# Kernel optimization log

Hardware: AMD Instinct MI355X
Metric: run time of the kernel (lower is better)

The kernel has to match this reference:

```python
import jax, jax.numpy as jnp
import numpy as np

SIGMA_D = 1.0  # init kwarg sigma_d
# d_model = 2 -> div_term = exp(arange(0,2,2) * (-ln(10000)/2)) = [1.0]


def setup_inputs() -> dict:
    key = jax.random.key(0)
    k0, k1 = jax.random.split(key)
    B, N, M = 4, 3000, 3000
    points0 = jax.random.normal(k0, (B, N, 2), dtype=jnp.float32)
    points1 = jax.random.normal(k1, (B, M, 2), dtype=jnp.float32)
    return {"points0": points0, "points1": points1}


def reference(points0, points1):
    # pairwise distance with points_normlize=True: sq_dist = clamp(2 - 2*<p0,p1>, 0)
    xy = jnp.einsum('bnc,bmc->bnm', points0, points1)  # (B,N,M)
    sq_dist = jnp.clip(2.0 - 2.0 * xy, 0.0)
    d_indices = jnp.sqrt(sq_dist) / SIGMA_D  # (B,N,M)
    # sinusoidal embedding with d_model=2, div_term=[1.0] -> [sin(d), cos(d)]
    d_embeddings = jnp.stack([jnp.sin(d_indices), jnp.cos(d_indices)], axis=-1)  # (B,N,M,2)
    d_embeddings = jax.lax.stop_gradient(d_embeddings)  # torch detaches + no_grad
    # einsum 'bnc,bnmc->bnc': multiply by sum over m
    points0_emb = points0 * d_embeddings.sum(axis=2)  # (B,N,2)
    # einsum 'bmc,bmnc->bmc' with permuted emb: sum over n
    points1_emb = points1 * d_embeddings.sum(axis=1)  # (B,M,2)
    return (points0_emb, points1_emb)
```

## Files before the change

### kernel.cpp

```cpp
#include <hip/hip_runtime.h>
#include <math.h>


#define GB 4
#define GN 3000
#define RB 32
#define BLKS 94
#define HALF 1500
#define K2 0.025330295910584444f
#define C2 0.050660591821168888f

#define COLPART_F2 (GB*BLKS*GN)

__device__ __forceinline__ float sreg(float x) {
    return __int_as_float(__builtin_amdgcn_readfirstlane(__float_as_int(x)));
}

__global__ __launch_bounds__(256, 4) void geo_pair_kernel(
    const float* __restrict__ p0,
    const float* __restrict__ p1,
    float2* __restrict__ ws)
{
    __shared__ float2 cp[4][768];

    const int lane = threadIdx.x & 63;
    const int wv   = threadIdx.x >> 6;
    const int h    = blockIdx.x & 1;
    const int t    = blockIdx.x >> 1;
    const int b    = t / BLKS;
    const int blk  = t - b * BLKS;
    const int row0 = blk * RB + wv * 8;
    const bool active = (row0 < GN);

    float s[8], c[8], ax[8], ay[8];
    float2 pr[8];
    #pragma unroll
    for (int r = 0; r < 8; ++r) {
        s[r] = 0.f; c[r] = 0.f; ax[r] = 0.f; ay[r] = 0.f;
        pr[r] = make_float2(0.f, 0.f);
    }
    const float2* __restrict__ qp = (const float2*)p1;
    float2 qA = make_float2(0.f, 0.f), qB = qA;
    const float c2v = C2;

    if (active) {
        const float2* ownp = (const float2*)p0 + b * GN + row0;
        const float mm = -2.0f * K2;
        #pragma unroll
        for (int r = 0; r < 8; ++r) {
            pr[r] = ownp[r];
            ax[r] = sreg(mm * pr[r].x);
            ay[r] = sreg(mm * pr[r].y);
        }
        qp = (const float2*)p1 + b * GN + h * HALF + lane;
        qA = qp[0];
        qB = qp[64];
    } else {
        for (int i = lane; i < 768; i += 64)
            cp[wv][i] = make_float2(0.f, 0.f);
    }

    float2* cw = &cp[wv][lane];

#define STEP(q) do {                                                         \
    float sn[8], cs[8];                                                      \
    _Pragma("unroll")                                                        \
    for (int r = 0; r < 8; ++r) {                                            \
        float tt = fmaf(ax[r], (q).x, fmaf(ay[r], (q).y, c2v));              \
        tt = fmaxf(tt, 0.f);                                                 \
        float rr = __builtin_amdgcn_sqrtf(tt);                               \
        sn[r] = __builtin_amdgcn_sinf(rr);                                   \
        cs[r] = __builtin_amdgcn_cosf(rr);                                   \
        s[r] += sn[r]; c[r] += cs[r];                                        \
    }                                                                        \
    float ssum = ((sn[0]+sn[1]) + (sn[2]+sn[3]))                             \
               + ((sn[4]+sn[5]) + (sn[6]+sn[7]));                            \
    float csum = ((cs[0]+cs[1]) + (cs[2]+cs[3]))                             \
               + ((cs[4]+cs[5]) + (cs[6]+cs[7]));                            \
    cw[0] = make_float2(ssum, csum);                                         \
    cw += 64;                                                                \
} while (0)

    if (active) {
        #pragma unroll 1
        for (int js = 0; js < 10; ++js) {
            float2 qC = qp[128];
            qp += 64;
            STEP(qA);
            qA = qB; qB = qC;
        }
        STEP(qA);
        STEP(qB);
        qA = qp[128];
        qB = qp[192];
        qp += 128;
    }
    __syncthreads();
    float2* __restrict__ dst = ws + (b * BLKS + blk) * GN + h * HALF;
    for (int i = threadIdx.x; i < 768; i += 256) {
        float2 a0 = cp[0][i], a1 = cp[1][i], a2 = cp[2][i], a3 = cp[3][i];
        dst[i] = make_float2((a0.x + a1.x) + (a2.x + a3.x),
                             (a0.y + a1.y) + (a2.y + a3.y));
    }
    __syncthreads();

    cw = &cp[wv][lane];
    if (active) {
        #pragma unroll 1
        for (int js = 0; js < 9; ++js) {
            float2 qC = qp[128];
            qp += 64;
            STEP(qA);
            qA = qB; qB = qC;
        }
        STEP(qA);
        STEP(qB);
        if (lane < 28) {
            float2 qT = qp[128];
            STEP(qT);
        }
    }
    __syncthreads();
    for (int i = threadIdx.x; i < 732; i += 256) {
        float2 a0 = cp[0][i], a1 = cp[1][i], a2 = cp[2][i], a3 = cp[3][i];
        dst[768 + i] = make_float2((a0.x + a1.x) + (a2.x + a3.x),
                                   (a0.y + a1.y) + (a2.y + a3.y));
    }
#undef STEP

    if (active) {
        #pragma unroll
        for (int off = 32; off >= 1; off >>= 1) {
            #pragma unroll
            for (int r = 0; r < 8; ++r) {
                s[r] += __shfl_down(s[r], off, 64);
                c[r] += __shfl_down(c[r], off, 64);
            }
        }
        if (lane == 0) {
            float2* rp = ws + COLPART_F2 + ((b * GN + row0) << 1) + h;
            #pragma unroll
            for (int r = 0; r < 8; ++r)
                rp[r * 2] = make_float2(s[r], c[r]);
        }
    }
}

__global__ __launch_bounds__(256, 4) void geo_reduce_kernel(
    const float* __restrict__ p0,
    const float* __restrict__ p1,
    const float2* __restrict__ ws,
    float2* __restrict__ out)
{
    __shared__ float2 acc[8][32];
    const int blk = blockIdx.x;
    if (blk < 375) {
        const int cc = threadIdx.x & 31;
        const int kc = threadIdx.x >> 5;
        const int g  = blk * 32 + cc;
        const int b  = g / GN;
        const int m  = g - b * GN;
        const float2* __restrict__ base = ws + b * (BLKS * GN) + m;
        const int k0 = kc * 12;
        float sv = 0.f, cv = 0.f;
        #pragma unroll
        for (int j = 0; j < 12; ++j) {
            const int k = k0 + j;
            if (k < BLKS) {
                float2 v = base[k * GN];
                sv += v.x; cv += v.y;
            }
        }
        acc[kc][cc] = make_float2(sv, cv);
        __syncthreads();
        if (kc == 0) {
            float2 r = acc[0][cc];
            #pragma unroll
            for (int j = 1; j < 8; ++j) { r.x += acc[j][cc].x; r.y += acc[j][cc].y; }
            const float2 p = ((const float2*)p1)[g];
            out[GB * GN + g] = make_float2(p.x * r.x, p.y * r.y);
        }
    } else {
        const int r = (blk - 375) * 256 + threadIdx.x;
        if (r < GB * GN) {
            const float2* rp = ws + COLPART_F2 + (r << 1);
            const float2 a = rp[0], d = rp[1];
            const float2 p = ((const float2*)p0)[r];
            out[r] = make_float2(p.x * (a.x + d.x), p.y * (a.y + d.y));
        }
    }
}

extern "C" void kernel_launch(void* const* d_in, const int* in_sizes, int n_in,
                              void* d_out, int out_size, void* d_ws, size_t ws_size,
                              hipStream_t stream) {
    const float* points0 = (const float*)d_in[0];
    const float* points1 = (const float*)d_in[1];

    geo_pair_kernel<<<dim3(GB * BLKS * 2), dim3(256), 0, stream>>>(
        points0, points1, (float2*)d_ws);
    geo_reduce_kernel<<<dim3(375 + 47), dim3(256), 0, stream>>>(
        points0, points1, (const float2*)d_ws, (float2*)d_out);
}
```

Baseline: 80.51 us.

## Write per-wave column partials directly to global, dropping LDS block reduction

Each wave now stores its per-column sin/cos partial sums straight to the workspace instead of combining the four waves of a block through shared memory with barriers. Inactive waves exit early. The reduce kernel now sums 375 row-group partials per column instead of 94. This removes the LDS traffic and syncthreads from the pair kernel, at the cost of about four times more workspace writes and reads in the reduction pass.

```diff
diff --git a/kernel.cpp b/kernel.cpp
--- a/kernel.cpp
+++ b/kernel.cpp
@@ -4,13 +4,13 @@
 
 #define GB 4
 #define GN 3000
-#define RB 32
+#define HALF 1500
+#define RGPB 375
 #define BLKS 94
-#define HALF 1500
 #define K2 0.025330295910584444f
 #define C2 0.050660591821168888f
 
-#define COLPART_F2 (GB*BLKS*GN)
+#define COLPART_F2 (GB*RGPB*GN)
 
 __device__ __forceinline__ float sreg(float x) {
     return __int_as_float(__builtin_amdgcn_readfirstlane(__float_as_int(x)));
@@ -21,48 +21,36 @@
     const float* __restrict__ p1,
     float2* __restrict__ ws)
 {
-    __shared__ float2 cp[4][768];
-
     const int lane = threadIdx.x & 63;
     const int wv   = threadIdx.x >> 6;
     const int h    = blockIdx.x & 1;
     const int t    = blockIdx.x >> 1;
     const int b    = t / BLKS;
     const int blk  = t - b * BLKS;
-    const int row0 = blk * RB + wv * 8;
-    const bool active = (row0 < GN);
+    const int rg   = blk * 4 + wv;
+    if (rg >= RGPB) return;
+    const int row0 = rg * 8;
 
     float s[8], c[8], ax[8], ay[8];
-    float2 pr[8];
-    #pragma unroll
-    for (int r = 0; r < 8; ++r) {
-        s[r] = 0.f; c[r] = 0.f; ax[r] = 0.f; ay[r] = 0.f;
-        pr[r] = make_float2(0.f, 0.f);
-    }
-    const float2* __restrict__ qp = (const float2*)p1;
-    float2 qA = make_float2(0.f, 0.f), qB = qA;
-    const float c2v = C2;
-
-    if (active) {
+    {
         const float2* ownp = (const float2*)p0 + b * GN + row0;
         const float mm = -2.0f * K2;
         #pragma unroll
         for (int r = 0; r < 8; ++r) {
-            pr[r] = ownp[r];
-            ax[r] = sreg(mm * pr[r].x);
-            ay[r] = sreg(mm * pr[r].y);
+            float2 pr = ownp[r];
+            ax[r] = sreg(mm * pr.x);
+            ay[r] = sreg(mm * pr.y);
+            s[r] = 0.f; c[r] = 0.f;
         }
-        qp = (const float2*)p1 + b * GN + h * HALF + lane;
-        qA = qp[0];
-        qB = qp[64];
-    } else {
-        for (int i = lane; i < 768; i += 64)
-            cp[wv][i] = make_float2(0.f, 0.f);
     }
+    const float c2v = C2;
 
-    float2* cw = &cp[wv][lane];
+    const float2* __restrict__ qp = (const float2*)p1 + b * GN + h * HALF + lane;
+    float2* __restrict__ sp = ws + (b * RGPB + rg) * GN + h * HALF + lane;
+    float2 qA = qp[0];
+    float2 qB = qp[64];
 
-#define STEP(q) do {                                                         \
+#define STEP(q, stoff) do {                                                  \
     float sn[8], cs[8];                                                      \
     _Pragma("unroll")                                                        \
     for (int r = 0; r < 8; ++r) {                                            \
@@ -77,72 +65,38 @@
                + ((sn[4]+sn[5]) + (sn[6]+sn[7]));                            \
     float csum = ((cs[0]+cs[1]) + (cs[2]+cs[3]))                             \
                + ((cs[4]+cs[5]) + (cs[6]+cs[7]));                            \
-    cw[0] = make_float2(ssum, csum);                                         \
-    cw += 64;                                                                \
+    sp[stoff] = make_float2(ssum, csum);                                     \
 } while (0)
 
-    if (active) {
-        #pragma unroll 1
-        for (int js = 0; js < 10; ++js) {
-            float2 qC = qp[128];
-            qp += 64;
-            STEP(qA);
-            qA = qB; qB = qC;
-        }
-        STEP(qA);
-        STEP(qB);
-        qA = qp[128];
-        qB = qp[192];
-        qp += 128;
+    #pragma unroll 1
+    for (int j = 0; j < 21; ++j) {
+        float2 qC = qp[128];
+        qp += 64;
+        STEP(qA, 0);
+        sp += 64;
+        qA = qB; qB = qC;
     }
-    __syncthreads();
-    float2* __restrict__ dst = ws + (b * BLKS + blk) * GN + h * HALF;
-    for (int i = threadIdx.x; i < 768; i += 256) {
-        float2 a0 = cp[0][i], a1 = cp[1][i], a2 = cp[2][i], a3 = cp[3][i];
-        dst[i] = make_float2((a0.x + a1.x) + (a2.x + a3.x),
-                             (a0.y + a1.y) + (a2.y + a3.y));
-    }
-    __syncthreads();
-
-    cw = &cp[wv][lane];
-    if (active) {
-        #pragma unroll 1
-        for (int js = 0; js < 9; ++js) {
-            float2 qC = qp[128];
-            qp += 64;
-            STEP(qA);
-            qA = qB; qB = qC;
-        }
-        STEP(qA);
-        STEP(qB);
-        if (lane < 28) {
-            float2 qT = qp[128];
-            STEP(qT);
-        }
-    }
-    __syncthreads();
-    for (int i = threadIdx.x; i < 732; i += 256) {
-        float2 a0 = cp[0][i], a1 = cp[1][i], a2 = cp[2][i], a3 = cp[3][i];
-        dst[768 + i] = make_float2((a0.x + a1.x) + (a2.x + a3.x),
-                                   (a0.y + a1.y) + (a2.y + a3.y));
+    STEP(qA, 0);
+    STEP(qB, 64);
+    if (lane < 28) {
+        float2 qT = qp[128];
+        STEP(qT, 128);
     }
 #undef STEP
 
-    if (active) {
+    #pragma unroll
+    for (int off = 32; off >= 1; off >>= 1) {
         #pragma unroll
-        for (int off = 32; off >= 1; off >>= 1) {
-            #pragma unroll
-            for (int r = 0; r < 8; ++r) {
-                s[r] += __shfl_down(s[r], off, 64);
-                c[r] += __shfl_down(c[r], off, 64);
-            }
+        for (int r = 0; r < 8; ++r) {
+            s[r] += __shfl_down(s[r], off, 64);
+            c[r] += __shfl_down(c[r], off, 64);
         }
-        if (lane == 0) {
-            float2* rp = ws + COLPART_F2 + ((b * GN + row0) << 1) + h;
-            #pragma unroll
-            for (int r = 0; r < 8; ++r)
-                rp[r * 2] = make_float2(s[r], c[r]);
-        }
+    }
+    if (lane == 0) {
+        float2* rp = ws + COLPART_F2 + ((b * GN + row0) << 1) + h;
+        #pragma unroll
+        for (int r = 0; r < 8; ++r)
+            rp[r * 2] = make_float2(s[r], c[r]);
     }
 }
 
@@ -160,13 +114,13 @@
         const int g  = blk * 32 + cc;
         const int b  = g / GN;
         const int m  = g - b * GN;
-        const float2* __restrict__ base = ws + b * (BLKS * GN) + m;
-        const int k0 = kc * 12;
+        const float2* __restrict__ base = ws + b * (RGPB * GN) + m;
+        const int k0 = kc * 47;
         float sv = 0.f, cv = 0.f;
         #pragma unroll
-        for (int j = 0; j < 12; ++j) {
+        for (int j = 0; j < 47; ++j) {
             const int k = k0 + j;
-            if (k < BLKS) {
+            if (k < RGPB) {
                 float2 v = base[k * GN];
                 sv += v.x; cv += v.y;
             }
```

Measured after the change: 97.86 us. +21.6%, slower.
